# Optimization experiments

Hardware: AMD Instinct MI355X
Metric: run time of the kernel (lower is better)

The kernel has to match this reference:

```python
import jax, jax.numpy as jnp
import numpy as np

N, D = 8192, 64


def setup_inputs() -> dict:
    key = jax.random.key(0)
    X = jax.random.normal(key, (N, D), dtype=jnp.float32)
    return {"X": X}


def reference(X):
    # Pairwise Euclidean distance matrix d_X[i, j] = ||X[i] - X[j]||_2.
    # Same math as sqrt(sum((X[:,None,:] - X[None,:,:])**2, -1)) but computed
    # via the Gram-matrix identity to avoid the [N, N, D] intermediate.
    sq_norms = jnp.sum(X * X, axis=1)                      # [N]
    gram = jnp.einsum('id,jd->ij', X, X)                   # [N, N]
    sq = sq_norms[:, None] + sq_norms[None, :] - 2.0 * gram
    sq = jnp.maximum(sq, 0.0)                              # clamp fp round-off
    # safe sqrt: exact zeros (diagonal) stay 0 with finite grad
    pos = sq > 0.0
    d_X = jnp.where(pos, jnp.sqrt(jnp.where(pos, sq, 1.0)), 0.0)
    return d_X
```

## Files before the change

kernel.cpp:

```cpp
#include <hip/hip_runtime.h>

#define NN 8192
#define DD 64

typedef short bf16x8 __attribute__((ext_vector_type(8)));
typedef float f32x4 __attribute__((ext_vector_type(4)));

__device__ __forceinline__ unsigned short f2bf(float f) {
    unsigned int u = __float_as_uint(f);
    unsigned int r = (u + 0x7FFFu + ((u >> 16) & 1u)) >> 16;
    return (unsigned short)r;
}

__global__ __launch_bounds__(256) void rips_setup(const float* __restrict__ X,
                                                  unsigned short* __restrict__ Xb,
                                                  float* __restrict__ norms) {
    const int t   = blockIdx.x * 256 + threadIdx.x;
    const int row = t >> 3;
    const int j   = t & 7;
    const float* p = X + (size_t)row * DD + j * 8;
    float4 lo = *(const float4*)p;
    float4 hi = *(const float4*)(p + 4);

    bf16x8 v;
    v[0] = (short)f2bf(lo.x); v[1] = (short)f2bf(lo.y);
    v[2] = (short)f2bf(lo.z); v[3] = (short)f2bf(lo.w);
    v[4] = (short)f2bf(hi.x); v[5] = (short)f2bf(hi.y);
    v[6] = (short)f2bf(hi.z); v[7] = (short)f2bf(hi.w);
    *(bf16x8*)(Xb + (size_t)row * DD + j * 8) = v;

    float acc = lo.x*lo.x + lo.y*lo.y + lo.z*lo.z + lo.w*lo.w
              + hi.x*hi.x + hi.y*hi.y + hi.z*hi.z + hi.w*hi.w;
    acc += __shfl_xor(acc, 1);
    acc += __shfl_xor(acc, 2);
    acc += __shfl_xor(acc, 4);
    if (j == 0) norms[row] = acc;
}

__global__ __launch_bounds__(256) void rips_main(const unsigned short* __restrict__ Xb,
                                                 const float* __restrict__ norms,
                                                 float* __restrict__ out) {
    const int rowBase = blockIdx.y * 128;
    const int colBase = blockIdx.x * 128;
    const int tid  = threadIdx.x;
    const int lane = tid & 63;
    const int w    = tid >> 6;
    const int wr   = w >> 1;
    const int wc   = w & 1;

    __shared__ float rn[128];
    __shared__ float cn[128];
    if (tid < 128) rn[tid]       = norms[rowBase + tid];
    else           cn[tid - 128] = norms[colBase + tid - 128];
    __syncthreads();

    const int fr = lane & 15;
    const int kg = lane >> 4;

    f32x4 acc[4][4];
    #pragma unroll
    for (int m = 0; m < 4; ++m)
        #pragma unroll
        for (int n = 0; n < 4; ++n)
            acc[m][n] = (f32x4){0.f, 0.f, 0.f, 0.f};

    #pragma unroll
    for (int kk = 0; kk < DD; kk += 32) {
        bf16x8 a[4], b[4];
        #pragma unroll
        for (int n = 0; n < 4; ++n)
            a[n] = *(const bf16x8*)(Xb + (size_t)(colBase + wc * 64 + n * 16 + fr) * DD + kk + kg * 8);
        #pragma unroll
        for (int m = 0; m < 4; ++m)
            b[m] = *(const bf16x8*)(Xb + (size_t)(rowBase + wr * 64 + m * 16 + fr) * DD + kk + kg * 8);
        #pragma unroll
        for (int m = 0; m < 4; ++m)
            #pragma unroll
            for (int n = 0; n < 4; ++n)
                acc[m][n] = __builtin_amdgcn_mfma_f32_16x16x32_bf16(a[n], b[m], acc[m][n], 0, 0, 0);
    }

    #pragma unroll
    for (int m = 0; m < 4; ++m) {
        const int row_l = wr * 64 + m * 16 + fr;
        const int grow  = rowBase + row_l;
        const float rnv = rn[row_l];
        #pragma unroll
        for (int n = 0; n < 4; ++n) {
            const int col0_l = wc * 64 + n * 16 + kg * 4;
            const int gcol0  = colBase + col0_l;
            const float4 cnv = *(const float4*)&cn[col0_l];
            float4 o;
            {
                float sq = fmaxf(rnv + cnv.x - 2.0f * acc[m][n][0], 0.0f);
                o.x = (grow == gcol0 + 0) ? 0.0f : sqrtf(sq);
                sq = fmaxf(rnv + cnv.y - 2.0f * acc[m][n][1], 0.0f);
                o.y = (grow == gcol0 + 1) ? 0.0f : sqrtf(sq);
                sq = fmaxf(rnv + cnv.z - 2.0f * acc[m][n][2], 0.0f);
                o.z = (grow == gcol0 + 2) ? 0.0f : sqrtf(sq);
                sq = fmaxf(rnv + cnv.w - 2.0f * acc[m][n][3], 0.0f);
                o.w = (grow == gcol0 + 3) ? 0.0f : sqrtf(sq);
            }
            *(float4*)(out + (size_t)grow * NN + gcol0) = o;
        }
    }
}

__global__ __launch_bounds__(256) void rips_fallback(const float* __restrict__ X,
                                                     float* __restrict__ out) {
    const int rowBase = blockIdx.y * 128;
    const int colBase = blockIdx.x * 128;
    const int tid  = threadIdx.x;
    const int lane = tid & 63;
    const int w    = tid >> 6;
    const int wr   = w >> 1;
    const int wc   = w & 1;

    __shared__ float rn[128];
    __shared__ float cn[128];
    {
        const int idx  = tid & 127;
        const int base = (tid < 128) ? rowBase : colBase;
        const float4* p = (const float4*)(X + (size_t)(base + idx) * DD);
        float acc = 0.0f;
        #pragma unroll
        for (int i = 0; i < 16; ++i) {
            float4 v = p[i];
            acc += v.x * v.x + v.y * v.y + v.z * v.z + v.w * v.w;
        }
        if (tid < 128) rn[idx] = acc;
        else           cn[idx] = acc;
    }
    __syncthreads();

    f32x4 acc[4][4];
    #pragma unroll
    for (int m = 0; m < 4; ++m)
        #pragma unroll
        for (int n = 0; n < 4; ++n)
            acc[m][n] = (f32x4){0.f, 0.f, 0.f, 0.f};

    const int fr = lane & 15;
    const int kg = lane >> 4;

    #pragma unroll
    for (int kk = 0; kk < DD; kk += 32) {
        bf16x8 a[4], b[4];
        #pragma unroll
        for (int m = 0; m < 4; ++m) {
            const float* p = X + (size_t)(rowBase + wr * 64 + m * 16 + fr) * DD + kk + kg * 8;
            float4 lo = *(const float4*)p;
            float4 hi = *(const float4*)(p + 4);
            bf16x8 t;
            t[0] = (short)f2bf(lo.x); t[1] = (short)f2bf(lo.y);
            t[2] = (short)f2bf(lo.z); t[3] = (short)f2bf(lo.w);
            t[4] = (short)f2bf(hi.x); t[5] = (short)f2bf(hi.y);
            t[6] = (short)f2bf(hi.z); t[7] = (short)f2bf(hi.w);
            a[m] = t;
        }
        #pragma unroll
        for (int n = 0; n < 4; ++n) {
            const float* p = X + (size_t)(colBase + wc * 64 + n * 16 + fr) * DD + kk + kg * 8;
            float4 lo = *(const float4*)p;
            float4 hi = *(const float4*)(p + 4);
            bf16x8 t;
            t[0] = (short)f2bf(lo.x); t[1] = (short)f2bf(lo.y);
            t[2] = (short)f2bf(lo.z); t[3] = (short)f2bf(lo.w);
            t[4] = (short)f2bf(hi.x); t[5] = (short)f2bf(hi.y);
            t[6] = (short)f2bf(hi.z); t[7] = (short)f2bf(hi.w);
            b[n] = t;
        }
        #pragma unroll
        for (int m = 0; m < 4; ++m)
            #pragma unroll
            for (int n = 0; n < 4; ++n)
                acc[m][n] = __builtin_amdgcn_mfma_f32_16x16x32_bf16(a[m], b[n], acc[m][n], 0, 0, 0);
    }

    #pragma unroll
    for (int m = 0; m < 4; ++m) {
        #pragma unroll
        for (int n = 0; n < 4; ++n) {
            #pragma unroll
            for (int r = 0; r < 4; ++r) {
                const int row_l = wr * 64 + m * 16 + kg * 4 + r;
                const int col_l = wc * 64 + n * 16 + fr;
                const float g  = acc[m][n][r];
                float sq = rn[row_l] + cn[col_l] - 2.0f * g;
                sq = fmaxf(sq, 0.0f);
                float dv = sqrtf(sq);
                const int grow = rowBase + row_l;
                const int gcol = colBase + col_l;
                if (grow == gcol) dv = 0.0f;
                out[(size_t)grow * NN + gcol] = dv;
            }
        }
    }
}

extern "C" void kernel_launch(void* const* d_in, const int* in_sizes, int n_in,
                              void* d_out, int out_size, void* d_ws, size_t ws_size,
                              hipStream_t stream) {
    const float* X = (const float*)d_in[0];
    float* out = (float*)d_out;

    const size_t xb_bytes   = (size_t)NN * DD * sizeof(unsigned short);
    const size_t norm_bytes = (size_t)NN * sizeof(float);

    if (ws_size >= xb_bytes + norm_bytes) {
        unsigned short* Xb = (unsigned short*)d_ws;
        float* norms = (float*)((char*)d_ws + xb_bytes);
        rips_setup<<<dim3(NN * 8 / 256, 1, 1), dim3(256, 1, 1), 0, stream>>>(X, Xb, norms);
        dim3 grid(NN / 128, NN / 128, 1);
        rips_main<<<grid, dim3(256, 1, 1), 0, stream>>>(Xb, norms, out);
    } else {
        dim3 grid(NN / 128, NN / 128, 1);
        rips_fallback<<<grid, dim3(256, 1, 1), 0, stream>>>(X, out);
    }
}
```

Baseline: 63.57 us.

## Compute only lower-triangular tiles and mirror results into transposed positions

Launches one block per lower-triangular 128x128 tile and decodes the tile coordinates from a linear block index with a square-root estimate. Each off-diagonal tile writes its result twice, once directly and once transposed, which halves the MFMA and epilogue work. The transposed writes are scalar, strided stores one row apart, so they coalesce poorly and the kernel is already bound by the output writes. It also switches to the hardware sqrt builtin, which may be slightly less precise than sqrtf.

```diff
diff --git a/kernel.cpp b/kernel.cpp
--- a/kernel.cpp
+++ b/kernel.cpp
@@ -10,6 +10,14 @@
     unsigned int u = __float_as_uint(f);
     unsigned int r = (u + 0x7FFFu + ((u >> 16) & 1u)) >> 16;
     return (unsigned short)r;
+}
+
+__device__ __forceinline__ float fsqrt(float x) {
+#if __has_builtin(__builtin_amdgcn_sqrtf)
+    return __builtin_amdgcn_sqrtf(x);
+#else
+    return sqrtf(x);
+#endif
 }
 
 __global__ __launch_bounds__(256) void rips_setup(const float* __restrict__ X,
@@ -37,11 +45,18 @@
     if (j == 0) norms[row] = acc;
 }
 
-__global__ __launch_bounds__(256) void rips_main(const unsigned short* __restrict__ Xb,
-                                                 const float* __restrict__ norms,
-                                                 float* __restrict__ out) {
-    const int rowBase = blockIdx.y * 128;
-    const int colBase = blockIdx.x * 128;
+__global__ __launch_bounds__(256) void rips_main_tri(const unsigned short* __restrict__ Xb,
+                                                     const float* __restrict__ norms,
+                                                     float* __restrict__ out) {
+    const int b = blockIdx.x;
+    int r = (int)((fsqrt(8.0f * (float)b + 1.0f) - 1.0f) * 0.5f);
+    while ((r + 1) * (r + 2) / 2 <= b) ++r;
+    while (r * (r + 1) / 2 > b) --r;
+    const int c = b - r * (r + 1) / 2;
+    const int rowBase = r * 128;
+    const int colBase = c * 128;
+    const bool isDiag = (r == c);
+
     const int tid  = threadIdx.x;
     const int lane = tid & 63;
     const int w    = tid >> 6;
@@ -66,18 +81,18 @@
 
     #pragma unroll
     for (int kk = 0; kk < DD; kk += 32) {
-        bf16x8 a[4], b[4];
+        bf16x8 a[4], bfr[4];
         #pragma unroll
         for (int n = 0; n < 4; ++n)
             a[n] = *(const bf16x8*)(Xb + (size_t)(colBase + wc * 64 + n * 16 + fr) * DD + kk + kg * 8);
         #pragma unroll
         for (int m = 0; m < 4; ++m)
-            b[m] = *(const bf16x8*)(Xb + (size_t)(rowBase + wr * 64 + m * 16 + fr) * DD + kk + kg * 8);
+            bfr[m] = *(const bf16x8*)(Xb + (size_t)(rowBase + wr * 64 + m * 16 + fr) * DD + kk + kg * 8);
         #pragma unroll
         for (int m = 0; m < 4; ++m)
             #pragma unroll
             for (int n = 0; n < 4; ++n)
-                acc[m][n] = __builtin_amdgcn_mfma_f32_16x16x32_bf16(a[n], b[m], acc[m][n], 0, 0, 0);
+                acc[m][n] = __builtin_amdgcn_mfma_f32_16x16x32_bf16(a[n], bfr[m], acc[m][n], 0, 0, 0);
     }
 
     #pragma unroll
@@ -91,17 +106,23 @@
             const int gcol0  = colBase + col0_l;
             const float4 cnv = *(const float4*)&cn[col0_l];
             float4 o;
-            {
-                float sq = fmaxf(rnv + cnv.x - 2.0f * acc[m][n][0], 0.0f);
-                o.x = (grow == gcol0 + 0) ? 0.0f : sqrtf(sq);
-                sq = fmaxf(rnv + cnv.y - 2.0f * acc[m][n][1], 0.0f);
-                o.y = (grow == gcol0 + 1) ? 0.0f : sqrtf(sq);
-                sq = fmaxf(rnv + cnv.z - 2.0f * acc[m][n][2], 0.0f);
-                o.z = (grow == gcol0 + 2) ? 0.0f : sqrtf(sq);
-                sq = fmaxf(rnv + cnv.w - 2.0f * acc[m][n][3], 0.0f);
-                o.w = (grow == gcol0 + 3) ? 0.0f : sqrtf(sq);
+            o.x = fsqrt(fmaxf(rnv + cnv.x - 2.0f * acc[m][n][0], 0.0f));
+            o.y = fsqrt(fmaxf(rnv + cnv.y - 2.0f * acc[m][n][1], 0.0f));
+            o.z = fsqrt(fmaxf(rnv + cnv.z - 2.0f * acc[m][n][2], 0.0f));
+            o.w = fsqrt(fmaxf(rnv + cnv.w - 2.0f * acc[m][n][3], 0.0f));
+            if (isDiag) {
+                if (grow == gcol0 + 0) o.x = 0.0f;
+                if (grow == gcol0 + 1) o.y = 0.0f;
+                if (grow == gcol0 + 2) o.z = 0.0f;
+                if (grow == gcol0 + 3) o.w = 0.0f;
             }
             *(float4*)(out + (size_t)grow * NN + gcol0) = o;
+            if (!isDiag) {
+                out[(size_t)(gcol0 + 0) * NN + grow] = o.x;
+                out[(size_t)(gcol0 + 1) * NN + grow] = o.y;
+                out[(size_t)(gcol0 + 2) * NN + grow] = o.z;
+                out[(size_t)(gcol0 + 3) * NN + grow] = o.w;
+            }
         }
     }
 }
@@ -211,8 +232,9 @@
         unsigned short* Xb = (unsigned short*)d_ws;
         float* norms = (float*)((char*)d_ws + xb_bytes);
         rips_setup<<<dim3(NN * 8 / 256, 1, 1), dim3(256, 1, 1), 0, stream>>>(X, Xb, norms);
-        dim3 grid(NN / 128, NN / 128, 1);
-        rips_main<<<grid, dim3(256, 1, 1), 0, stream>>>(Xb, norms, out);
+        const int ntiles = NN / 128;
+        const int nblocks = ntiles * (ntiles + 1) / 2;
+        rips_main_tri<<<dim3(nblocks, 1, 1), dim3(256, 1, 1), 0, stream>>>(Xb, norms, out);
     } else {
         dim3 grid(NN / 128, NN / 128, 1);
         rips_fallback<<<grid, dim3(256, 1, 1), 0, stream>>>(X, out);
```

New measurement: 62.55 us. Within noise of the previous version (-1.6%).
